# Performance work log

Hardware: AMD Instinct MI355X
Metric: run time of the kernel (lower is better)

The kernel has to match this reference:

```python
import jax, jax.numpy as jnp
import numpy as np

N_NODES = 20000
N_EDGES = 320000
IN_C = 128
H0, H1 = 256, 256
OUT_C = 64


def _glorot(key, shape):
    lim = float(np.sqrt(6.0 / (shape[0] + shape[1])))
    return jax.random.uniform(key, shape, jnp.float32, -lim, lim)


def setup_inputs() -> dict:
    key = jax.random.key(0)
    ks = jax.random.split(key, 16)
    x = jax.random.normal(ks[0], (N_NODES, IN_C), jnp.float32)
    edge_index = jax.random.randint(ks[1], (2, N_EDGES), 0, N_NODES, jnp.int64)
    return {
        "x": x,
        "edge_index": edge_index,
        # conv1: in -> h0
        "W1l": _glorot(ks[2], (IN_C, H0)), "b1": jnp.zeros((H0,), jnp.float32), "W1r": _glorot(ks[3], (IN_C, H0)),
        # conv_list[0]: h0 -> h1
        "W2l": _glorot(ks[4], (H0, H1)), "b2": jnp.zeros((H1,), jnp.float32), "W2r": _glorot(ks[5], (H0, H1)),
        # initial residual: in -> h1
        "Wres": _glorot(ks[6], (IN_C, H1)), "bres": jnp.zeros((H1,), jnp.float32),
        # conv_mu: h1 -> out
        "Wmul": _glorot(ks[7], (H1, OUT_C)), "bmu": jnp.zeros((OUT_C,), jnp.float32), "Wmur": _glorot(ks[8], (H1, OUT_C)),
        # conv_logstd: h1 -> out
        "Wlsl": _glorot(ks[9], (H1, OUT_C)), "bls": jnp.zeros((OUT_C,), jnp.float32), "Wlsr": _glorot(ks[10], (H1, OUT_C)),
    }


def _sage(x, src, dst, Wl, b, Wr):
    """PyG SAGEConv with mean aggregation: lin_l(mean_j x_j) + lin_r(x_i)."""
    n = x.shape[0]
    msgs = x[src]                                             # [E, d] gather
    s = jax.ops.segment_sum(msgs, dst, num_segments=n)        # [N, d]
    deg = jax.ops.segment_sum(jnp.ones((src.shape[0],), x.dtype), dst, num_segments=n)
    agg = s / jnp.maximum(deg, 1.0)[:, None]
    return agg @ Wl + b + x @ Wr


def reference(x, edge_index, W1l, b1, W1r, W2l, b2, W2r, Wres, bres,
              Wmul, bmu, Wmur, Wlsl, bls, Wlsr):
    src, dst = edge_index[0], edge_index[1]
    h = jax.nn.relu(_sage(x, src, dst, W1l, b1, W1r))
    h = jax.nn.relu(_sage(h, src, dst, W2l, b2, W2r)) + (x @ Wres + bres)
    mu = _sage(h, src, dst, Wmul, bmu, Wmur)
    logstd = _sage(h, src, dst, Wlsl, bls, Wlsr)
    return mu, logstd
```

## Files before the change

### kernel.cpp

```cpp
#include <hip/hip_runtime.h>
#include <cstddef>

#define NN 20000
#define NE 320000

typedef short bf16x8 __attribute__((ext_vector_type(8)));
typedef float f32x4 __attribute__((ext_vector_type(4)));
typedef unsigned short u16;

__device__ __forceinline__ float bf2f(u16 u) {
    unsigned x = ((unsigned)u) << 16;
    return __builtin_bit_cast(float, x);
}
__device__ __forceinline__ u16 f2bf(float f) {
    unsigned x = __builtin_bit_cast(unsigned, f);
    x = (x + 0x7fff + ((x >> 16) & 1)) >> 16;
    return (u16)x;
}

__global__ __launch_bounds__(256) void detect_kernel(const void* __restrict__ edges, int* flag) {
    __shared__ int bad;
    if (threadIdx.x == 0) bad = 0;
    __syncthreads();
    int any = 0;
    for (int i = blockIdx.x * 256 + threadIdx.x; i < NE; i += 64 * 256) {
        long long v = ((const long long*)edges)[i];
        if (v < 0 || v >= NN) any = 1;
    }
    if (any) bad = 1;
    __syncthreads();
    if (threadIdx.x == 0 && bad) atomicOr(flag, 1);
}

__global__ __launch_bounds__(256) void convert_kernel(const void* __restrict__ edges,
                                                      const int* __restrict__ flag,
                                                      int* __restrict__ src, int* __restrict__ dst,
                                                      int* __restrict__ deg) {
    int i = blockIdx.x * blockDim.x + threadIdx.x;
    if (i >= NE) return;
    int s, d;
    if (*flag) {
        s = ((const int*)edges)[i];
        d = ((const int*)edges)[NE + i];
    } else {
        s = (int)((const long long*)edges)[i];
        d = (int)((const long long*)edges)[NE + i];
    }
    src[i] = s;
    dst[i] = d;
    atomicAdd(&deg[d], 1);
}

__global__ __launch_bounds__(256) void scan1_kernel(const int* __restrict__ deg,
                                                    int* __restrict__ incl, int* __restrict__ bsum) {
    __shared__ int buf[256];
    int t = threadIdx.x, i = blockIdx.x * 256 + t;
    int v = (i < NN) ? deg[i] : 0;
    buf[t] = v;
    __syncthreads();
    for (int off = 1; off < 256; off <<= 1) {
        int u = (t >= off) ? buf[t - off] : 0;
        __syncthreads();
        buf[t] += u;
        __syncthreads();
    }
    if (i < NN) incl[i] = buf[t];
    if (t == 255) bsum[blockIdx.x] = buf[255];
}

__global__ __launch_bounds__(256) void scan2_kernel(const int* __restrict__ bsum,
                                                    int* __restrict__ boff) {
    __shared__ int buf[256];
    const int nb = (NN + 255) / 256;
    int t = threadIdx.x;
    int v = (t < nb) ? bsum[t] : 0;
    buf[t] = v;
    __syncthreads();
    for (int off = 1; off < 256; off <<= 1) {
        int u = (t >= off) ? buf[t - off] : 0;
        __syncthreads();
        buf[t] += u;
        __syncthreads();
    }
    if (t < nb) boff[t] = buf[t] - v;
}

__global__ __launch_bounds__(256) void scan3_kernel(const int* __restrict__ deg,
                                                    const int* __restrict__ incl,
                                                    const int* __restrict__ boff,
                                                    int* __restrict__ rowptr) {
    int i = blockIdx.x * 256 + threadIdx.x;
    if (i < NN) rowptr[i] = boff[i >> 8] + incl[i] - deg[i];
    if (i == NN) rowptr[NN] = NE;
}

__global__ __launch_bounds__(256) void fill_kernel(const int* __restrict__ src,
                                                   const int* __restrict__ dst,
                                                   const int* __restrict__ rowptr,
                                                   int* __restrict__ cursor,
                                                   int* __restrict__ csr_src) {
    int i = blockIdx.x * blockDim.x + threadIdx.x;
    if (i >= NE) return;
    int d = dst[i];
    int p = atomicAdd(&cursor[d], 1);
    csr_src[rowptr[d] + p] = src[i];
}

__global__ __launch_bounds__(256) void cast_kernel(const float* __restrict__ in,
                                                   u16* __restrict__ out, int n4) {
    int i = blockIdx.x * 256 + threadIdx.x;
    if (i >= n4) return;
    float4 v = *(const float4*)(in + (size_t)i * 4);
    ushort4 o;
    o.x = f2bf(v.x); o.y = f2bf(v.y); o.z = f2bf(v.z); o.w = f2bf(v.w);
    *(ushort4*)(out + (size_t)i * 4) = o;
}

struct WJobs {
    const float* W[9];
    u16* WT[9];
    int K[9];
    int N[9];
};
__global__ __launch_bounds__(256) void wtrans_all(WJobs jobs) {
    int y = blockIdx.y;
    int K = jobs.K[y], N = jobs.N[y];
    int i = blockIdx.x * 256 + threadIdx.x;
    if (i >= K * N) return;
    int k = i / N, n = i % N;
    jobs.WT[y][(size_t)n * K + k] = f2bf(jobs.W[y][i]);
}

template <int D>
__global__ __launch_bounds__(256) void aggregate_kernel(const u16* __restrict__ feat,
                                                        const int* __restrict__ csr_src,
                                                        const int* __restrict__ rowptr,
                                                        u16* __restrict__ out) {
    int node = blockIdx.x * 4 + (threadIdx.x >> 6);
    if (node >= NN) return;
    int lane = threadIdx.x & 63;
    int beg = rowptr[node], end = rowptr[node + 1];
    int cnt = end - beg;
    float inv = 1.0f / (float)(cnt > 0 ? cnt : 1);

    constexpr int NSUB = (D == 256) ? 2 : 4;
    constexpr int LPG = 64 / NSUB;
    int sub = lane / LPG;
    int c8 = lane % LPG;
    const u16* fc = feat + c8 * 8;

    float a0[8] = {0.f,0.f,0.f,0.f,0.f,0.f,0.f,0.f};
    float a1[8] = {0.f,0.f,0.f,0.f,0.f,0.f,0.f,0.f};

    int e = beg + sub;
    for (; e + 3 * NSUB < end; e += 4 * NSUB) {
        int s0 = csr_src[e];
        int s1 = csr_src[e + NSUB];
        int s2 = csr_src[e + 2 * NSUB];
        int s3 = csr_src[e + 3 * NSUB];
        bf16x8 u0 = *(const bf16x8*)(fc + (size_t)s0 * D);
        bf16x8 u1 = *(const bf16x8*)(fc + (size_t)s1 * D);
        bf16x8 u2 = *(const bf16x8*)(fc + (size_t)s2 * D);
        bf16x8 u3 = *(const bf16x8*)(fc + (size_t)s3 * D);
#pragma unroll
        for (int j = 0; j < 8; j++) {
            a0[j] += bf2f((u16)u0[j]) + bf2f((u16)u2[j]);
            a1[j] += bf2f((u16)u1[j]) + bf2f((u16)u3[j]);
        }
    }
    for (; e < end; e += NSUB) {
        int s = csr_src[e];
        bf16x8 u = *(const bf16x8*)(fc + (size_t)s * D);
#pragma unroll
        for (int j = 0; j < 8; j++) a0[j] += bf2f((u16)u[j]);
    }
#pragma unroll
    for (int j = 0; j < 8; j++) {
        a0[j] += a1[j];
        if (NSUB == 4) a0[j] += __shfl_xor(a0[j], 16);
        a0[j] += __shfl_xor(a0[j], 32);
    }
    if (sub == 0) {
        bf16x8 o;
#pragma unroll
        for (int j = 0; j < 8; j++) o[j] = (short)f2bf(a0[j] * inv);
        *(bf16x8*)(out + (size_t)node * D + c8 * 8) = o;
    }
}

template <int KS0, int KS1, int KS2, int RELU01, int SPLIT, int OUT_F32, int NWAVES>
__global__ __launch_bounds__(NWAVES * 64) void gemm_lds(
    const u16* __restrict__ A0, const u16* __restrict__ B0T,
    const u16* __restrict__ A1, const u16* __restrict__ B1T,
    const u16* __restrict__ A2, const u16* __restrict__ B2T,
    const float* __restrict__ bias, const float* __restrict__ bias2,
    void* __restrict__ Cout, void* __restrict__ Cout2, int M) {
    constexpr int NT = NWAVES * 64;
    constexpr int NCOL = NWAVES * 64;
    constexpr int AI = 4096 / (NT * 16);
    constexpr int BI = (NCOL * 64) / (NT * 16);
    constexpr int TOT = KS0 + KS1 + KS2;
    constexpr int pS1 = KS0, pS2 = KS0 + KS1;
    constexpr int BOFF = 64 * 32;
    constexpr int BUFSZ = BOFF + NCOL * 32;

    __shared__ __align__(16) u16 smem[2][BUFSZ];

    const int t = threadIdx.x;
    const int w = t >> 6, l = t & 63;
    const int l15 = l & 15, lhi = l >> 4;
    const int rowBase = blockIdx.x * 64;
    const int wc = w * 64;
    const int srow = t >> 2, skk = t & 3;

    f32x4 acc[4][4];
#pragma unroll
    for (int r = 0; r < 4; r++)
#pragma unroll
        for (int n = 0; n < 4; n++) acc[r][n] = f32x4{0.f, 0.f, 0.f, 0.f};

    bf16x8 ar[AI], br[BI];

    auto gload = [&](const u16* __restrict__ A, const u16* __restrict__ BT, int K, int ko) {
#pragma unroll
        for (int i = 0; i < AI; i++) {
            int row = rowBase + i * (NT / 4) + srow;
            row = row < M ? row : M - 1;
            ar[i] = *(const bf16x8*)(A + (size_t)row * K + ko + skk * 8);
        }
#pragma unroll
        for (int i = 0; i < BI; i++) {
            int n = i * (NT / 4) + srow;
            br[i] = *(const bf16x8*)(BT + (size_t)n * K + ko + skk * 8);
        }
    };
    auto swrite = [&](int buf) {
        u16* base = smem[buf];
#pragma unroll
        for (int i = 0; i < AI; i++)
            *(bf16x8*)(base + (size_t)(i * NT + t) * 8) = ar[i];
#pragma unroll
        for (int i = 0; i < BI; i++)
            *(bf16x8*)(base + BOFF + (size_t)(i * NT + t) * 8) = br[i];
    };

    gload(A0, B0T, KS0 * 32, 0);
    int cur = 0;

#pragma unroll 1
    for (int step = 0; step < TOT; step++) {
        __syncthreads();
        swrite(cur);
        int ns = step + 1;
        if (ns < TOT) {
            if (KS2 > 0 && ns >= pS2)  gload(A2, B2T, KS2 * 32, (ns - pS2) * 32);
            else if (ns >= pS1)        gload(A1, B1T, KS1 * 32, (ns - pS1) * 32);
            else                       gload(A0, B0T, KS0 * 32, ns * 32);
        }
        __syncthreads();
        const u16* sb = smem[cur];
        bf16x8 af[4], bf[4];
#pragma unroll
        for (int r = 0; r < 4; r++)
            af[r] = *(const bf16x8*)(sb + (r * 16 + l15) * 32 + lhi * 8);
#pragma unroll
        for (int n = 0; n < 4; n++)
            bf[n] = *(const bf16x8*)(sb + BOFF + (wc + n * 16 + l15) * 32 + lhi * 8);
#pragma unroll
        for (int r = 0; r < 4; r++)
#pragma unroll
            for (int n = 0; n < 4; n++)
                acc[r][n] = __builtin_amdgcn_mfma_f32_16x16x32_bf16(af[r], bf[n], acc[r][n], 0, 0, 0);
        if (RELU01 && step == pS2 - 1) {
#pragma unroll
            for (int n = 0; n < 4; n++) {
                float b = bias[wc + n * 16 + l15];
#pragma unroll
                for (int r = 0; r < 4; r++)
#pragma unroll
                    for (int j = 0; j < 4; j++)
                        acc[r][n][j] = fmaxf(acc[r][n][j] + b, 0.f);
            }
        }
        cur ^= 1;
    }

#pragma unroll
    for (int n = 0; n < 4; n++) {
        int col = wc + n * 16 + l15;
        float badd;
        if constexpr (SPLIT)        badd = (col < 64) ? bias[col] : bias2[col - 64];
        else if constexpr (KS2 > 0) badd = bias2[col];
        else if constexpr (RELU01)  badd = 0.f;
        else                        badd = bias[col];
#pragma unroll
        for (int r = 0; r < 4; r++) {
#pragma unroll
            for (int j = 0; j < 4; j++) {
                int row = rowBase + r * 16 + lhi * 4 + j;
                if (row >= M) continue;
                float v = acc[r][n][j] + badd;
                if constexpr (SPLIT) {
                    if (col < 64) ((float*)Cout)[(size_t)row * 64 + col] = v;
                    else          ((float*)Cout2)[(size_t)row * 64 + (col - 64)] = v;
                } else if constexpr (OUT_F32) {
                    ((float*)Cout)[(size_t)row * NCOL + col] = v;
                } else {
                    ((u16*)Cout)[(size_t)row * NCOL + col] = f2bf(v);
                }
            }
        }
    }
}

extern "C" void kernel_launch(void* const* d_in, const int* in_sizes, int n_in,
                              void* d_out, int out_size, void* d_ws, size_t ws_size,
                              hipStream_t stream) {
    const float* x    = (const float*)d_in[0];
    const void*  edges = d_in[1];
    const float* W1l  = (const float*)d_in[2];
    const float* b1   = (const float*)d_in[3];
    const float* W1r  = (const float*)d_in[4];
    const float* W2l  = (const float*)d_in[5];
    const float* b2   = (const float*)d_in[6];
    const float* W2r  = (const float*)d_in[7];
    const float* Wres = (const float*)d_in[8];
    const float* bres = (const float*)d_in[9];
    const float* Wmul = (const float*)d_in[10];
    const float* bmu  = (const float*)d_in[11];
    const float* Wmur = (const float*)d_in[12];
    const float* Wlsl = (const float*)d_in[13];
    const float* bls  = (const float*)d_in[14];
    const float* Wlsr = (const float*)d_in[15];
    float* out = (float*)d_out;

    char* ws = (char*)d_ws;
    size_t off = 0;
    int* flag    = (int*)(ws + off); off += 256;
    int* src     = (int*)(ws + off); off += (size_t)NE * 4;
    int* dst     = (int*)(ws + off); off += (size_t)NE * 4;
    int* csr_src = (int*)(ws + off); off += (size_t)NE * 4;
    int* deg     = (int*)(ws + off); off += (size_t)NN * 4;
    int* rowptr  = (int*)(ws + off); off += (size_t)(NN + 8) * 4;
    int* cursor  = (int*)(ws + off); off += (size_t)NN * 4;
    int* incl    = (int*)(ws + off); off += (size_t)NN * 4;
    int* bsum    = (int*)(ws + off); off += 256 * 4;
    int* boff    = (int*)(ws + off); off += 256 * 4;
    off = (off + 255) & ~(size_t)255;
    u16* xb    = (u16*)(ws + off); off += (size_t)NN * 128 * 2;
    u16* agg1b = (u16*)(ws + off); off += (size_t)NN * 128 * 2;
    u16* h1b   = (u16*)(ws + off); off += (size_t)NN * 256 * 2;
    u16* h2b   = (u16*)(ws + off); off += (size_t)NN * 256 * 2;
    u16* aggb  = (u16*)(ws + off); off += (size_t)NN * 256 * 2;
    u16* W1lT  = (u16*)(ws + off); off += 128 * 256 * 2;
    u16* W1rT  = (u16*)(ws + off); off += 128 * 256 * 2;
    u16* W2lT  = (u16*)(ws + off); off += 256 * 256 * 2;
    u16* W2rT  = (u16*)(ws + off); off += 256 * 256 * 2;
    u16* WresT = (u16*)(ws + off); off += 128 * 256 * 2;
    u16* WcatL = (u16*)(ws + off); off += 128 * 256 * 2;
    u16* WcatR = (u16*)(ws + off); off += 128 * 256 * 2;

    hipMemsetAsync(flag, 0, 4, stream);
    hipMemsetAsync(deg, 0, (size_t)NN * 4, stream);
    hipMemsetAsync(cursor, 0, (size_t)NN * 4, stream);

    const int SB = (NN + 255) / 256;

    detect_kernel<<<64, 256, 0, stream>>>(edges, flag);
    convert_kernel<<<NE / 256, 256, 0, stream>>>(edges, flag, src, dst, deg);
    scan1_kernel<<<SB, 256, 0, stream>>>(deg, incl, bsum);
    scan2_kernel<<<1, 256, 0, stream>>>(bsum, boff);
    scan3_kernel<<<SB, 256, 0, stream>>>(deg, incl, boff, rowptr);
    fill_kernel<<<NE / 256, 256, 0, stream>>>(src, dst, rowptr, cursor, csr_src);

    cast_kernel<<<(NN * 128 / 4 + 255) / 256, 256, 0, stream>>>(x, xb, NN * 128 / 4);

    WJobs jobs;
    jobs.W[0] = W1l;  jobs.WT[0] = W1lT;            jobs.K[0] = 128; jobs.N[0] = 256;
    jobs.W[1] = W1r;  jobs.WT[1] = W1rT;            jobs.K[1] = 128; jobs.N[1] = 256;
    jobs.W[2] = W2l;  jobs.WT[2] = W2lT;            jobs.K[2] = 256; jobs.N[2] = 256;
    jobs.W[3] = W2r;  jobs.WT[3] = W2rT;            jobs.K[3] = 256; jobs.N[3] = 256;
    jobs.W[4] = Wres; jobs.WT[4] = WresT;           jobs.K[4] = 128; jobs.N[4] = 256;
    jobs.W[5] = Wmul; jobs.WT[5] = WcatL;           jobs.K[5] = 256; jobs.N[5] = 64;
    jobs.W[6] = Wlsl; jobs.WT[6] = WcatL + 64*256;  jobs.K[6] = 256; jobs.N[6] = 64;
    jobs.W[7] = Wmur; jobs.WT[7] = WcatR;           jobs.K[7] = 256; jobs.N[7] = 64;
    jobs.W[8] = Wlsr; jobs.WT[8] = WcatR + 64*256;  jobs.K[8] = 256; jobs.N[8] = 64;
    wtrans_all<<<dim3(256, 9), 256, 0, stream>>>(jobs);

    const int GB = (NN + 63) / 64;

    aggregate_kernel<128><<<NN / 4, 256, 0, stream>>>(xb, csr_src, rowptr, agg1b);
    gemm_lds<4, 4, 0, 1, 0, 0, 4><<<GB, 256, 0, stream>>>(
        agg1b, W1lT, xb, W1rT, nullptr, nullptr, b1, nullptr, h1b, nullptr, NN);

    aggregate_kernel<256><<<NN / 4, 256, 0, stream>>>(h1b, csr_src, rowptr, aggb);
    gemm_lds<8, 8, 4, 1, 0, 0, 4><<<GB, 256, 0, stream>>>(
        aggb, W2lT, h1b, W2rT, xb, WresT, b2, bres, h2b, nullptr, NN);

    aggregate_kernel<256><<<NN / 4, 256, 0, stream>>>(h2b, csr_src, rowptr, aggb);
    gemm_lds<8, 8, 0, 0, 1, 1, 2><<<GB, 128, 0, stream>>>(
        aggb, WcatL, h2b, WcatR, nullptr, nullptr, bmu, bls, out, out + (size_t)NN * 64, NN);
}
```

Measured before the change: 184.1 us.

## Project final layer before aggregation to shrink gathered feature width

The final mu/logstd SAGE layer now runs the linear projection first (h2 times concatenated Wl|Wr into a 256-wide bf16 buffer), then a new aggregation kernel gathers only the 128 left-projected columns, averages them, and adds the right-projected self term and bias. This exploits linearity of mean aggregation so the neighbor gather reads half as many bytes per edge as gathering 256-wide h2. It also merges the three memsets into one contiguous memset. The trade-off is an extra 256-wide bf16 intermediate write and read, plus bf16 rounding of the projected values before the sum.

```diff
diff --git a/kernel.cpp b/kernel.cpp
--- a/kernel.cpp
+++ b/kernel.cpp
@@ -188,13 +188,78 @@
     }
 }
 
-template <int KS0, int KS1, int KS2, int RELU01, int SPLIT, int OUT_F32, int NWAVES>
+__global__ __launch_bounds__(256) void agg_final(const u16* __restrict__ R,
+                                                 const int* __restrict__ csr_src,
+                                                 const int* __restrict__ rowptr,
+                                                 const float* __restrict__ bmu,
+                                                 const float* __restrict__ bls,
+                                                 float* __restrict__ out) {
+    int node = blockIdx.x * 4 + (threadIdx.x >> 6);
+    if (node >= NN) return;
+    int lane = threadIdx.x & 63;
+    int beg = rowptr[node], end = rowptr[node + 1];
+    int cnt = end - beg;
+    float inv = 1.0f / (float)(cnt > 0 ? cnt : 1);
+
+    int sub = lane >> 4;
+    int c8 = lane & 15;
+    const u16* fc = R + c8 * 8;
+
+    float a0[8] = {0.f,0.f,0.f,0.f,0.f,0.f,0.f,0.f};
+    float a1[8] = {0.f,0.f,0.f,0.f,0.f,0.f,0.f,0.f};
+
+    int e = beg + sub;
+    for (; e + 12 < end; e += 16) {
+        int s0 = csr_src[e];
+        int s1 = csr_src[e + 4];
+        int s2 = csr_src[e + 8];
+        int s3 = csr_src[e + 12];
+        bf16x8 u0 = *(const bf16x8*)(fc + (size_t)s0 * 256);
+        bf16x8 u1 = *(const bf16x8*)(fc + (size_t)s1 * 256);
+        bf16x8 u2 = *(const bf16x8*)(fc + (size_t)s2 * 256);
+        bf16x8 u3 = *(const bf16x8*)(fc + (size_t)s3 * 256);
+#pragma unroll
+        for (int j = 0; j < 8; j++) {
+            a0[j] += bf2f((u16)u0[j]) + bf2f((u16)u2[j]);
+            a1[j] += bf2f((u16)u1[j]) + bf2f((u16)u3[j]);
+        }
+    }
+    for (; e < end; e += 4) {
+        int s = csr_src[e];
+        bf16x8 u = *(const bf16x8*)(fc + (size_t)s * 256);
+#pragma unroll
+        for (int j = 0; j < 8; j++) a0[j] += bf2f((u16)u[j]);
+    }
+#pragma unroll
+    for (int j = 0; j < 8; j++) {
+        a0[j] += a1[j];
+        a0[j] += __shfl_xor(a0[j], 16);
+        a0[j] += __shfl_xor(a0[j], 32);
+    }
+    if (sub == 0) {
+        int c0 = c8 * 8;
+        bf16x8 q = *(const bf16x8*)(R + (size_t)node * 256 + 128 + c0);
+        float o[8];
+#pragma unroll
+        for (int j = 0; j < 8; j++) {
+            int c = c0 + j;
+            float b = (c < 64) ? bmu[c] : bls[c - 64];
+            o[j] = a0[j] * inv + bf2f((u16)q[j]) + b;
+        }
+        float* dst = (c0 < 64) ? (out + (size_t)node * 64 + c0)
+                               : (out + (size_t)NN * 64 + (size_t)node * 64 + (c0 - 64));
+        *(float4*)dst = make_float4(o[0], o[1], o[2], o[3]);
+        *(float4*)(dst + 4) = make_float4(o[4], o[5], o[6], o[7]);
+    }
+}
+
+template <int KS0, int KS1, int KS2, int RELU01, int OUT_F32, int NWAVES>
 __global__ __launch_bounds__(NWAVES * 64) void gemm_lds(
     const u16* __restrict__ A0, const u16* __restrict__ B0T,
     const u16* __restrict__ A1, const u16* __restrict__ B1T,
     const u16* __restrict__ A2, const u16* __restrict__ B2T,
     const float* __restrict__ bias, const float* __restrict__ bias2,
-    void* __restrict__ Cout, void* __restrict__ Cout2, int M) {
+    void* __restrict__ Cout, int M) {
     constexpr int NT = NWAVES * 64;
     constexpr int NCOL = NWAVES * 64;
     constexpr int AI = 4096 / (NT * 16);
@@ -253,9 +318,9 @@
         swrite(cur);
         int ns = step + 1;
         if (ns < TOT) {
-            if (KS2 > 0 && ns >= pS2)  gload(A2, B2T, KS2 * 32, (ns - pS2) * 32);
-            else if (ns >= pS1)        gload(A1, B1T, KS1 * 32, (ns - pS1) * 32);
-            else                       gload(A0, B0T, KS0 * 32, ns * 32);
+            if (KS2 > 0 && ns >= pS2)       gload(A2, B2T, KS2 * 32, (ns - pS2) * 32);
+            else if (KS1 > 0 && ns >= pS1)  gload(A1, B1T, KS1 * 32, (ns - pS1) * 32);
+            else                            gload(A0, B0T, KS0 * 32, ns * 32);
         }
         __syncthreads();
         const u16* sb = smem[cur];
@@ -289,8 +354,7 @@
     for (int n = 0; n < 4; n++) {
         int col = wc + n * 16 + l15;
         float badd;
-        if constexpr (SPLIT)        badd = (col < 64) ? bias[col] : bias2[col - 64];
-        else if constexpr (KS2 > 0) badd = bias2[col];
+        if constexpr (KS2 > 0)      badd = bias2[col];
         else if constexpr (RELU01)  badd = 0.f;
         else                        badd = bias[col];
 #pragma unroll
@@ -300,10 +364,7 @@
                 int row = rowBase + r * 16 + lhi * 4 + j;
                 if (row >= M) continue;
                 float v = acc[r][n][j] + badd;
-                if constexpr (SPLIT) {
-                    if (col < 64) ((float*)Cout)[(size_t)row * 64 + col] = v;
-                    else          ((float*)Cout2)[(size_t)row * 64 + (col - 64)] = v;
-                } else if constexpr (OUT_F32) {
+                if constexpr (OUT_F32) {
                     ((float*)Cout)[(size_t)row * NCOL + col] = v;
                 } else {
                     ((u16*)Cout)[(size_t)row * NCOL + col] = f2bf(v);
@@ -336,13 +397,15 @@
 
     char* ws = (char*)d_ws;
     size_t off = 0;
-    int* flag    = (int*)(ws + off); off += 256;
+    int*   flag   = (int*)(ws + off); off += 256;
+    int*   deg    = (int*)(ws + off); off += (size_t)NN * 4;
+    int*   cursor = (int*)(ws + off); off += (size_t)NN * 4;
+    float* zerosf = (float*)(ws + off); off += 1024;
+    const size_t zlen = off;
     int* src     = (int*)(ws + off); off += (size_t)NE * 4;
     int* dst     = (int*)(ws + off); off += (size_t)NE * 4;
     int* csr_src = (int*)(ws + off); off += (size_t)NE * 4;
-    int* deg     = (int*)(ws + off); off += (size_t)NN * 4;
     int* rowptr  = (int*)(ws + off); off += (size_t)(NN + 8) * 4;
-    int* cursor  = (int*)(ws + off); off += (size_t)NN * 4;
     int* incl    = (int*)(ws + off); off += (size_t)NN * 4;
     int* bsum    = (int*)(ws + off); off += 256 * 4;
     int* boff    = (int*)(ws + off); off += 256 * 4;
@@ -352,17 +415,15 @@
     u16* h1b   = (u16*)(ws + off); off += (size_t)NN * 256 * 2;
     u16* h2b   = (u16*)(ws + off); off += (size_t)NN * 256 * 2;
     u16* aggb  = (u16*)(ws + off); off += (size_t)NN * 256 * 2;
+    u16* Rb    = (u16*)(ws + off); off += (size_t)NN * 256 * 2;
     u16* W1lT  = (u16*)(ws + off); off += 128 * 256 * 2;
     u16* W1rT  = (u16*)(ws + off); off += 128 * 256 * 2;
     u16* W2lT  = (u16*)(ws + off); off += 256 * 256 * 2;
     u16* W2rT  = (u16*)(ws + off); off += 256 * 256 * 2;
     u16* WresT = (u16*)(ws + off); off += 128 * 256 * 2;
-    u16* WcatL = (u16*)(ws + off); off += 128 * 256 * 2;
-    u16* WcatR = (u16*)(ws + off); off += 128 * 256 * 2;
-
-    hipMemsetAsync(flag, 0, 4, stream);
-    hipMemsetAsync(deg, 0, (size_t)NN * 4, stream);
-    hipMemsetAsync(cursor, 0, (size_t)NN * 4, stream);
+    u16* Wcat  = (u16*)(ws + off); off += 256 * 256 * 2;
+
+    hipMemsetAsync(flag, 0, zlen, stream);
 
     const int SB = (NN + 255) / 256;
 
@@ -376,28 +437,28 @@
     cast_kernel<<<(NN * 128 / 4 + 255) / 256, 256, 0, stream>>>(x, xb, NN * 128 / 4);
 
     WJobs jobs;
-    jobs.W[0] = W1l;  jobs.WT[0] = W1lT;            jobs.K[0] = 128; jobs.N[0] = 256;
-    jobs.W[1] = W1r;  jobs.WT[1] = W1rT;            jobs.K[1] = 128; jobs.N[1] = 256;
-    jobs.W[2] = W2l;  jobs.WT[2] = W2lT;            jobs.K[2] = 256; jobs.N[2] = 256;
-    jobs.W[3] = W2r;  jobs.WT[3] = W2rT;            jobs.K[3] = 256; jobs.N[3] = 256;
-    jobs.W[4] = Wres; jobs.WT[4] = WresT;           jobs.K[4] = 128; jobs.N[4] = 256;
-    jobs.W[5] = Wmul; jobs.WT[5] = WcatL;           jobs.K[5] = 256; jobs.N[5] = 64;
-    jobs.W[6] = Wlsl; jobs.WT[6] = WcatL + 64*256;  jobs.K[6] = 256; jobs.N[6] = 64;
-    jobs.W[7] = Wmur; jobs.WT[7] = WcatR;           jobs.K[7] = 256; jobs.N[7] = 64;
-    jobs.W[8] = Wlsr; jobs.WT[8] = WcatR + 64*256;  jobs.K[8] = 256; jobs.N[8] = 64;
+    jobs.W[0] = W1l;  jobs.WT[0] = W1lT;           jobs.K[0] = 128; jobs.N[0] = 256;
+    jobs.W[1] = W1r;  jobs.WT[1] = W1rT;           jobs.K[1] = 128; jobs.N[1] = 256;
+    jobs.W[2] = W2l;  jobs.WT[2] = W2lT;           jobs.K[2] = 256; jobs.N[2] = 256;
+    jobs.W[3] = W2r;  jobs.WT[3] = W2rT;           jobs.K[3] = 256; jobs.N[3] = 256;
+    jobs.W[4] = Wres; jobs.WT[4] = WresT;          jobs.K[4] = 128; jobs.N[4] = 256;
+    jobs.W[5] = Wmul; jobs.WT[5] = Wcat;           jobs.K[5] = 256; jobs.N[5] = 64;
+    jobs.W[6] = Wlsl; jobs.WT[6] = Wcat + 64*256;  jobs.K[6] = 256; jobs.N[6] = 64;
+    jobs.W[7] = Wmur; jobs.WT[7] = Wcat + 128*256; jobs.K[7] = 256; jobs.N[7] = 64;
+    jobs.W[8] = Wlsr; jobs.WT[8] = Wcat + 192*256; jobs.K[8] = 256; jobs.N[8] = 64;
     wtrans_all<<<dim3(256, 9), 256, 0, stream>>>(jobs);
 
     const int GB = (NN + 63) / 64;
 
     aggregate_kernel<128><<<NN / 4, 256, 0, stream>>>(xb, csr_src, rowptr, agg1b);
-    gemm_lds<4, 4, 0, 1, 0, 0, 4><<<GB, 256, 0, stream>>>(
-        agg1b, W1lT, xb, W1rT, nullptr, nullptr, b1, nullptr, h1b, nullptr, NN);
+    gemm_lds<4, 4, 0, 1, 0, 4><<<GB, 256, 0, stream>>>(
+        agg1b, W1lT, xb, W1rT, nullptr, nullptr, b1, nullptr, h1b, NN);
 
     aggregate_kernel<256><<<NN / 4, 256, 0, stream>>>(h1b, csr_src, rowptr, aggb);
-    gemm_lds<8, 8, 4, 1, 0, 0, 4><<<GB, 256, 0, stream>>>(
-        aggb, W2lT, h1b, W2rT, xb, WresT, b2, bres, h2b, nullptr, NN);
-
-    aggregate_kernel<256><<<NN / 4, 256, 0, stream>>>(h2b, csr_src, rowptr, aggb);
-    gemm_lds<8, 8, 0, 0, 1, 1, 2><<<GB, 128, 0, stream>>>(
-        aggb, WcatL, h2b, WcatR, nullptr, nullptr, bmu, bls, out, out + (size_t)NN * 64, NN);
-}
+    gemm_lds<8, 8, 4, 1, 0, 4><<<GB, 256, 0, stream>>>(
+        aggb, W2lT, h1b, W2rT, xb, WresT, b2, bres, h2b, NN);
+
+    gemm_lds<8, 0, 0, 0, 0, 4><<<GB, 256, 0, stream>>>(
+        h2b, Wcat, nullptr, nullptr, nullptr, nullptr, zerosf, nullptr, Rb, NN);
+    agg_final<<<NN / 4, 256, 0, stream>>>(Rb, csr_src, rowptr, bmu, bls, out);
+}
```

Measured after the change: 173.2 us, median of 2. 5.9% less time.
